# Performance work log

Hardware: AMD Instinct MI355X
Metric: run time of the kernel (lower is better)

## Reference

```python
import jax, jax.numpy as jnp
import numpy as np

BOUND = 1.0
GRID = 128
DENSITY_SCALE = 1.0
DENSITY_THRESH = 0.01
T_THRESH = 1e-3
BG_COLOR = 1.0
N_RAYS = 65536
N_STEPS = 128


def setup_inputs() -> dict:
    key = jax.random.key(0)
    ks = jax.random.split(key, 7)
    N, S = N_RAYS, N_STEPS
    # ray origins inside the AABB, directions unit-norm
    rays_o = (jax.random.uniform(ks[0], (N, 3)) - 0.5) * 1.0
    d = jax.random.normal(ks[1], (N, 3))
    rays_d = d / jnp.linalg.norm(d, axis=-1, keepdims=True)
    sigmas = jax.random.uniform(ks[2], (N, S)) * 2.0      # raw densities at samples
    rgbs = jax.random.uniform(ks[3], (N, S, 3))           # albedo at samples
    sun_v = jax.random.uniform(ks[4], (N, S))             # sun visibility (shadow)
    sky_color = jax.random.uniform(ks[5], (N, S, 3))      # ambient sky color
    nears = jnp.full((N,), 0.2, dtype=jnp.float32)
    fars = jnp.full((N,), 2.0, dtype=jnp.float32)
    density_grid = jax.random.uniform(ks[6], (GRID, GRID, GRID))  # occupancy grid
    return dict(rays_o=rays_o, rays_d=rays_d, sigmas=sigmas, rgbs=rgbs,
                sun_v=sun_v, sky_color=sky_color, nears=nears, fars=fars,
                density_grid=density_grid)


def reference(rays_o, rays_d, sigmas, rgbs, sun_v, sky_color, nears, fars, density_grid):
    N, S = sigmas.shape
    # --- march: uniform samples in [near, far] (dt_gamma = 0) ---
    dt = (fars - nears) / S                                        # [N]
    t = nears[:, None] + (jnp.arange(S, dtype=sigmas.dtype) + 0.5) * dt[:, None]  # [N,S]
    xyz = rays_o[:, None, :] + t[..., None] * rays_d[:, None, :]   # [N,S,3]
    # --- occupancy-grid lookup (density_bitfield test) ---
    idx = jnp.clip(((xyz + BOUND) / (2.0 * BOUND) * GRID).astype(jnp.int32), 0, GRID - 1)
    occ = density_grid[idx[..., 0], idx[..., 1], idx[..., 2]] > DENSITY_THRESH  # [N,S]
    inside = jnp.all(jnp.abs(xyz) < BOUND, axis=-1)                # AABB clip
    sig = jnp.where(occ & inside, sigmas * DENSITY_SCALE, 0.0)     # skip empty space
    # --- shading: irradiance = sun_v + (1 - sun_v) * sky_color ---
    irr = sun_v[..., None] + (1.0 - sun_v[..., None]) * sky_color  # [N,S,3]
    rgb = rgbs * irr
    # --- alpha compositing with early termination ---
    tau = sig * dt[:, None]                                        # optical depth per step
    T = jnp.exp(-(jnp.cumsum(tau, axis=-1) - tau))                 # exclusive transmittance
    alpha = 1.0 - jnp.exp(-tau)
    w = jnp.where(T > T_THRESH, alpha * T, 0.0)                    # early-termination mask
    weights_sum = w.sum(-1)                                        # [N]
    depth = (w * t).sum(-1)                                        # [N]
    image = jnp.einsum('ns,nsc->nc', w, rgb) + (1.0 - weights_sum)[:, None] * BG_COLOR
    depth = jnp.clip(depth - nears, 0.0) / (fars - nears)
    return image, depth, weights_sum
```

## Files before the change

kernel.cpp:

```cpp
#include <hip/hip_runtime.h>


#define NRAYS  65536
#define NSTEPS 128
#define GRIDN  128

typedef float v2f __attribute__((ext_vector_type(2)));

__global__ __launch_bounds__(256, 4) void nerf_render_kernel(
    const float* __restrict__ rays_o,
    const float* __restrict__ rays_d,
    const float* __restrict__ sigmas,
    const float* __restrict__ rgbs,
    const float* __restrict__ sun_v,
    const float* __restrict__ sky,
    const float* __restrict__ nears,
    const float* __restrict__ fars,
    const float* __restrict__ grid,
    float* __restrict__ out)
{
    const int tid  = blockIdx.x * blockDim.x + threadIdx.x;
    const int ray  = tid >> 6;
    const int lane = threadIdx.x & 63;
    if (ray >= NRAYS) return;

    const float nearv = nears[ray];
    const float farv  = fars[ray];
    const float dt    = (farv - nearv) * (1.0f / NSTEPS);

    const float ox = rays_o[ray * 3 + 0];
    const float oy = rays_o[ray * 3 + 1];
    const float oz = rays_o[ray * 3 + 2];
    const float dx = rays_d[ray * 3 + 0];
    const float dy = rays_d[ray * 3 + 1];
    const float dz = rays_d[ray * 3 + 2];

    const int  s0   = 2 * lane;
    const long base = (long)ray * NSTEPS + s0;

    const v2f sg  = *(const v2f*)(sigmas + base);
    const v2f sv  = *(const v2f*)(sun_v  + base);
    const v2f r01 = *(const v2f*)(rgbs + base * 3);
    const v2f r23 = *(const v2f*)(rgbs + base * 3 + 2);
    const v2f r45 = *(const v2f*)(rgbs + base * 3 + 4);
    const v2f k01 = *(const v2f*)(sky  + base * 3);
    const v2f k23 = *(const v2f*)(sky  + base * 3 + 2);
    const v2f k45 = *(const v2f*)(sky  + base * 3 + 4);

    float t_[2], tau_[2], cr_[2], cg_[2], cb_[2];
    const float rr_[2] = { r01[0], r23[1] };
    const float rg_[2] = { r01[1], r45[0] };
    const float rb_[2] = { r23[0], r45[1] };
    const float kr_[2] = { k01[0], k23[1] };
    const float kg_[2] = { k01[1], k45[0] };
    const float kb_[2] = { k23[0], k45[1] };

    #pragma unroll
    for (int j = 0; j < 2; ++j) {
        const int s = s0 + j;
        const float t = __fadd_rn(nearv, __fmul_rn((float)s + 0.5f, dt));
        const float x = __fadd_rn(ox, __fmul_rn(t, dx));
        const float y = __fadd_rn(oy, __fmul_rn(t, dy));
        const float z = __fadd_rn(oz, __fmul_rn(t, dz));

        int ix = (int)__fmul_rn(__fadd_rn(x, 1.0f), 64.0f);
        int iy = (int)__fmul_rn(__fadd_rn(y, 1.0f), 64.0f);
        int iz = (int)__fmul_rn(__fadd_rn(z, 1.0f), 64.0f);
        ix = min(max(ix, 0), GRIDN - 1);
        iy = min(max(iy, 0), GRIDN - 1);
        iz = min(max(iz, 0), GRIDN - 1);
        const float g = grid[((long)ix * GRIDN + iy) * GRIDN + iz];

        const bool inside = (fabsf(x) < 1.0f) & (fabsf(y) < 1.0f) & (fabsf(z) < 1.0f);
        const bool occ    = (g > 0.01f) & inside;

        const float sig = occ ? sg[j] : 0.0f;

        const float s_v = sv[j];
        cr_[j] = rr_[j] * (s_v + (1.0f - s_v) * kr_[j]);
        cg_[j] = rg_[j] * (s_v + (1.0f - s_v) * kg_[j]);
        cb_[j] = rb_[j] * (s_v + (1.0f - s_v) * kb_[j]);

        t_[j]   = t;
        tau_[j] = sig * dt;
    }

    const float pair = tau_[0] + tau_[1];
    float incl = pair;
    #pragma unroll
    for (int off = 1; off < 64; off <<= 1) {
        const float u = __shfl_up(incl, off);
        if (lane >= off) incl += u;
    }
    const float eLane = incl - pair;
    const float excl_[2] = { eLane, eLane + tau_[0] };

    float wsum = 0.0f, dsum = 0.0f, ir = 0.0f, ig = 0.0f, ib = 0.0f;
    #pragma unroll
    for (int j = 0; j < 2; ++j) {
        const float T     = expf(-excl_[j]);
        const float alpha = 1.0f - expf(-tau_[j]);
        const float w     = (T > 1e-3f) ? alpha * T : 0.0f;
        wsum += w; dsum += w * t_[j];
        ir += w * cr_[j]; ig += w * cg_[j]; ib += w * cb_[j];
    }

    #pragma unroll
    for (int off = 32; off > 0; off >>= 1) {
        wsum += __shfl_xor(wsum, off);
        dsum += __shfl_xor(dsum, off);
        ir   += __shfl_xor(ir, off);
        ig   += __shfl_xor(ig, off);
        ib   += __shfl_xor(ib, off);
    }

    if (lane == 0) {
        const float bgw = 1.0f - wsum;
        out[ray * 3 + 0] = ir + bgw;
        out[ray * 3 + 1] = ig + bgw;
        out[ray * 3 + 2] = ib + bgw;
        out[3 * NRAYS + ray] = fmaxf(dsum - nearv, 0.0f) / (farv - nearv);
        out[4 * NRAYS + ray] = wsum;
    }
}

extern "C" void kernel_launch(void* const* d_in, const int* in_sizes, int n_in,
                              void* d_out, int out_size, void* d_ws, size_t ws_size,
                              hipStream_t stream) {
    const float* rays_o = (const float*)d_in[0];
    const float* rays_d = (const float*)d_in[1];
    const float* sigmas = (const float*)d_in[2];
    const float* rgbs   = (const float*)d_in[3];
    const float* sun_v  = (const float*)d_in[4];
    const float* sky    = (const float*)d_in[5];
    const float* nears  = (const float*)d_in[6];
    const float* fars   = (const float*)d_in[7];
    const float* grid   = (const float*)d_in[8];
    float* out = (float*)d_out;

    const int threads = 256;
    const int blocks  = (NRAYS * 64) / threads;
    nerf_render_kernel<<<blocks, threads, 0, stream>>>(
        rays_o, rays_d, sigmas, rgbs, sun_v, sky, nears, fars, grid, out);
}
```

Measured before the change: 289.0 us.

## Process eight rays per wave with double-buffered prefetch and nontemporal loads

Each wave now handles eight consecutive rays instead of one, with A/B register sets so loads for the next ray (including the grid gather) are issued before compositing the current one. Streaming per-sample inputs use nontemporal loads to avoid polluting cache. This cuts the block count by 8x and is meant to hide memory latency via software pipelining, at the cost of more registers per thread and less wave-level parallelism.

```diff
diff --git a/kernel.cpp b/kernel.cpp
--- a/kernel.cpp
+++ b/kernel.cpp
@@ -4,8 +4,109 @@
 #define NRAYS  65536
 #define NSTEPS 128
 #define GRIDN  128
+#define RPW    8
+#define WPB    4
 
 typedef float v2f __attribute__((ext_vector_type(2)));
+
+__device__ __forceinline__ v2f ntload2(const float* p) {
+    return __builtin_nontemporal_load((const v2f*)p);
+}
+
+#define PREFETCH(rayi, P)                                                      \
+  do {                                                                         \
+    const int _ray = (rayi);                                                   \
+    P##_near = nears[_ray];  P##_far = fars[_ray];                             \
+    P##_ox = rays_o[_ray*3+0]; P##_oy = rays_o[_ray*3+1]; P##_oz = rays_o[_ray*3+2]; \
+    P##_dx = rays_d[_ray*3+0]; P##_dy = rays_d[_ray*3+1]; P##_dz = rays_d[_ray*3+2]; \
+    const float _dt = (P##_far - P##_near) * (1.0f/NSTEPS);                    \
+    _Pragma("unroll")                                                          \
+    for (int _j = 0; _j < 2; ++_j) {                                           \
+      const float _t = __fadd_rn(P##_near, __fmul_rn((float)(s0+_j)+0.5f, _dt)); \
+      const float _x = __fadd_rn(P##_ox, __fmul_rn(_t, P##_dx));               \
+      const float _y = __fadd_rn(P##_oy, __fmul_rn(_t, P##_dy));               \
+      const float _z = __fadd_rn(P##_oz, __fmul_rn(_t, P##_dz));               \
+      int _ix = (int)__fmul_rn(__fadd_rn(_x, 1.0f), 64.0f);                    \
+      int _iy = (int)__fmul_rn(__fadd_rn(_y, 1.0f), 64.0f);                    \
+      int _iz = (int)__fmul_rn(__fadd_rn(_z, 1.0f), 64.0f);                    \
+      _ix = min(max(_ix,0),GRIDN-1); _iy = min(max(_iy,0),GRIDN-1); _iz = min(max(_iz,0),GRIDN-1); \
+      const float _g = grid[((long)_ix*GRIDN + _iy)*GRIDN + _iz];              \
+      if (_j == 0) P##_g0 = _g; else P##_g1 = _g;                              \
+    }                                                                          \
+    const long _base = (long)_ray * NSTEPS + s0;                               \
+    P##_sg  = ntload2(sigmas + _base);                                         \
+    P##_sv  = ntload2(sun_v  + _base);                                         \
+    P##_r01 = ntload2(rgbs + _base*3);                                         \
+    P##_r23 = ntload2(rgbs + _base*3 + 2);                                     \
+    P##_r45 = ntload2(rgbs + _base*3 + 4);                                     \
+    P##_k01 = ntload2(sky  + _base*3);                                         \
+    P##_k23 = ntload2(sky  + _base*3 + 2);                                     \
+    P##_k45 = ntload2(sky  + _base*3 + 4);                                     \
+  } while (0)
+
+#define COMPUTE(rayi, P)                                                       \
+  do {                                                                         \
+    const int _ray = (rayi);                                                   \
+    const float _dt = (P##_far - P##_near) * (1.0f/NSTEPS);                    \
+    float t_[2], tau_[2], cr_[2], cg_[2], cb_[2];                              \
+    const float rr_[2] = { P##_r01[0], P##_r23[1] };                           \
+    const float rg_[2] = { P##_r01[1], P##_r45[0] };                           \
+    const float rb_[2] = { P##_r23[0], P##_r45[1] };                           \
+    const float kr_[2] = { P##_k01[0], P##_k23[1] };                           \
+    const float kg_[2] = { P##_k01[1], P##_k45[0] };                           \
+    const float kb_[2] = { P##_k23[0], P##_k45[1] };                           \
+    const float g_[2]  = { P##_g0, P##_g1 };                                   \
+    _Pragma("unroll")                                                          \
+    for (int _j = 0; _j < 2; ++_j) {                                           \
+      const float _t = __fadd_rn(P##_near, __fmul_rn((float)(s0+_j)+0.5f, _dt)); \
+      const float _x = __fadd_rn(P##_ox, __fmul_rn(_t, P##_dx));               \
+      const float _y = __fadd_rn(P##_oy, __fmul_rn(_t, P##_dy));               \
+      const float _z = __fadd_rn(P##_oz, __fmul_rn(_t, P##_dz));               \
+      const bool _inside = (fabsf(_x) < 1.0f) & (fabsf(_y) < 1.0f) & (fabsf(_z) < 1.0f); \
+      const bool _occ    = (g_[_j] > 0.01f) & _inside;                         \
+      const float _sig = _occ ? P##_sg[_j] : 0.0f;                             \
+      const float _sv  = P##_sv[_j];                                           \
+      cr_[_j] = rr_[_j] * (_sv + (1.0f - _sv) * kr_[_j]);                      \
+      cg_[_j] = rg_[_j] * (_sv + (1.0f - _sv) * kg_[_j]);                      \
+      cb_[_j] = rb_[_j] * (_sv + (1.0f - _sv) * kb_[_j]);                      \
+      t_[_j]   = _t;                                                           \
+      tau_[_j] = _sig * _dt;                                                   \
+    }                                                                          \
+    const float _pair = tau_[0] + tau_[1];                                     \
+    float _incl = _pair;                                                       \
+    _Pragma("unroll")                                                          \
+    for (int _off = 1; _off < 64; _off <<= 1) {                                \
+      const float _u = __shfl_up(_incl, _off);                                 \
+      if (lane >= _off) _incl += _u;                                           \
+    }                                                                          \
+    const float _eLane = _incl - _pair;                                        \
+    const float excl_[2] = { _eLane, _eLane + tau_[0] };                       \
+    float _ws = 0.0f, _ds = 0.0f, _ir = 0.0f, _ig = 0.0f, _ib = 0.0f;          \
+    _Pragma("unroll")                                                          \
+    for (int _j = 0; _j < 2; ++_j) {                                           \
+      const float _T     = expf(-excl_[_j]);                                   \
+      const float _alpha = 1.0f - expf(-tau_[_j]);                             \
+      const float _w     = (_T > 1e-3f) ? _alpha * _T : 0.0f;                  \
+      _ws += _w; _ds += _w * t_[_j];                                           \
+      _ir += _w * cr_[_j]; _ig += _w * cg_[_j]; _ib += _w * cb_[_j];           \
+    }                                                                          \
+    _Pragma("unroll")                                                          \
+    for (int _off = 32; _off > 0; _off >>= 1) {                                \
+      _ws += __shfl_xor(_ws, _off);                                            \
+      _ds += __shfl_xor(_ds, _off);                                            \
+      _ir += __shfl_xor(_ir, _off);                                            \
+      _ig += __shfl_xor(_ig, _off);                                            \
+      _ib += __shfl_xor(_ib, _off);                                            \
+    }                                                                          \
+    if (lane == 0) {                                                           \
+      const float _bgw = 1.0f - _ws;                                           \
+      out[_ray*3 + 0] = _ir + _bgw;                                            \
+      out[_ray*3 + 1] = _ig + _bgw;                                            \
+      out[_ray*3 + 2] = _ib + _bgw;                                            \
+      out[3*NRAYS + _ray] = fmaxf(_ds - P##_near, 0.0f) / (P##_far - P##_near);\
+      out[4*NRAYS + _ray] = _ws;                                               \
+    }                                                                          \
+  } while (0)
 
 __global__ __launch_bounds__(256, 4) void nerf_render_kernel(
     const float* __restrict__ rays_o,
@@ -19,109 +120,26 @@
     const float* __restrict__ grid,
     float* __restrict__ out)
 {
-    const int tid  = blockIdx.x * blockDim.x + threadIdx.x;
-    const int ray  = tid >> 6;
     const int lane = threadIdx.x & 63;
-    if (ray >= NRAYS) return;
+    const int wloc = __builtin_amdgcn_readfirstlane(threadIdx.x >> 6);
+    const int wave = blockIdx.x * WPB + wloc;
+    const int ray0 = wave * RPW;
+    const int s0   = 2 * lane;
 
-    const float nearv = nears[ray];
-    const float farv  = fars[ray];
-    const float dt    = (farv - nearv) * (1.0f / NSTEPS);
+    v2f A_sg, A_sv, A_r01, A_r23, A_r45, A_k01, A_k23, A_k45;
+    float A_g0, A_g1, A_near, A_far, A_ox, A_oy, A_oz, A_dx, A_dy, A_dz;
+    v2f B_sg, B_sv, B_r01, B_r23, B_r45, B_k01, B_k23, B_k45;
+    float B_g0, B_g1, B_near, B_far, B_ox, B_oy, B_oz, B_dx, B_dy, B_dz;
 
-    const float ox = rays_o[ray * 3 + 0];
-    const float oy = rays_o[ray * 3 + 1];
-    const float oz = rays_o[ray * 3 + 2];
-    const float dx = rays_d[ray * 3 + 0];
-    const float dy = rays_d[ray * 3 + 1];
-    const float dz = rays_d[ray * 3 + 2];
-
-    const int  s0   = 2 * lane;
-    const long base = (long)ray * NSTEPS + s0;
-
-    const v2f sg  = *(const v2f*)(sigmas + base);
-    const v2f sv  = *(const v2f*)(sun_v  + base);
-    const v2f r01 = *(const v2f*)(rgbs + base * 3);
-    const v2f r23 = *(const v2f*)(rgbs + base * 3 + 2);
-    const v2f r45 = *(const v2f*)(rgbs + base * 3 + 4);
-    const v2f k01 = *(const v2f*)(sky  + base * 3);
-    const v2f k23 = *(const v2f*)(sky  + base * 3 + 2);
-    const v2f k45 = *(const v2f*)(sky  + base * 3 + 4);
-
-    float t_[2], tau_[2], cr_[2], cg_[2], cb_[2];
-    const float rr_[2] = { r01[0], r23[1] };
-    const float rg_[2] = { r01[1], r45[0] };
-    const float rb_[2] = { r23[0], r45[1] };
-    const float kr_[2] = { k01[0], k23[1] };
-    const float kg_[2] = { k01[1], k45[0] };
-    const float kb_[2] = { k23[0], k45[1] };
-
-    #pragma unroll
-    for (int j = 0; j < 2; ++j) {
-        const int s = s0 + j;
-        const float t = __fadd_rn(nearv, __fmul_rn((float)s + 0.5f, dt));
-        const float x = __fadd_rn(ox, __fmul_rn(t, dx));
-        const float y = __fadd_rn(oy, __fmul_rn(t, dy));
-        const float z = __fadd_rn(oz, __fmul_rn(t, dz));
-
-        int ix = (int)__fmul_rn(__fadd_rn(x, 1.0f), 64.0f);
-        int iy = (int)__fmul_rn(__fadd_rn(y, 1.0f), 64.0f);
-        int iz = (int)__fmul_rn(__fadd_rn(z, 1.0f), 64.0f);
-        ix = min(max(ix, 0), GRIDN - 1);
-        iy = min(max(iy, 0), GRIDN - 1);
-        iz = min(max(iz, 0), GRIDN - 1);
-        const float g = grid[((long)ix * GRIDN + iy) * GRIDN + iz];
-
-        const bool inside = (fabsf(x) < 1.0f) & (fabsf(y) < 1.0f) & (fabsf(z) < 1.0f);
-        const bool occ    = (g > 0.01f) & inside;
-
-        const float sig = occ ? sg[j] : 0.0f;
-
-        const float s_v = sv[j];
-        cr_[j] = rr_[j] * (s_v + (1.0f - s_v) * kr_[j]);
-        cg_[j] = rg_[j] * (s_v + (1.0f - s_v) * kg_[j]);
-        cb_[j] = rb_[j] * (s_v + (1.0f - s_v) * kb_[j]);
-
-        t_[j]   = t;
-        tau_[j] = sig * dt;
-    }
-
-    const float pair = tau_[0] + tau_[1];
-    float incl = pair;
-    #pragma unroll
-    for (int off = 1; off < 64; off <<= 1) {
-        const float u = __shfl_up(incl, off);
-        if (lane >= off) incl += u;
-    }
-    const float eLane = incl - pair;
-    const float excl_[2] = { eLane, eLane + tau_[0] };
-
-    float wsum = 0.0f, dsum = 0.0f, ir = 0.0f, ig = 0.0f, ib = 0.0f;
-    #pragma unroll
-    for (int j = 0; j < 2; ++j) {
-        const float T     = expf(-excl_[j]);
-        const float alpha = 1.0f - expf(-tau_[j]);
-        const float w     = (T > 1e-3f) ? alpha * T : 0.0f;
-        wsum += w; dsum += w * t_[j];
-        ir += w * cr_[j]; ig += w * cg_[j]; ib += w * cb_[j];
-    }
-
-    #pragma unroll
-    for (int off = 32; off > 0; off >>= 1) {
-        wsum += __shfl_xor(wsum, off);
-        dsum += __shfl_xor(dsum, off);
-        ir   += __shfl_xor(ir, off);
-        ig   += __shfl_xor(ig, off);
-        ib   += __shfl_xor(ib, off);
-    }
-
-    if (lane == 0) {
-        const float bgw = 1.0f - wsum;
-        out[ray * 3 + 0] = ir + bgw;
-        out[ray * 3 + 1] = ig + bgw;
-        out[ray * 3 + 2] = ib + bgw;
-        out[3 * NRAYS + ray] = fmaxf(dsum - nearv, 0.0f) / (farv - nearv);
-        out[4 * NRAYS + ray] = wsum;
-    }
+    PREFETCH(ray0 + 0, A);
+    PREFETCH(ray0 + 1, B);  COMPUTE(ray0 + 0, A);
+    PREFETCH(ray0 + 2, A);  COMPUTE(ray0 + 1, B);
+    PREFETCH(ray0 + 3, B);  COMPUTE(ray0 + 2, A);
+    PREFETCH(ray0 + 4, A);  COMPUTE(ray0 + 3, B);
+    PREFETCH(ray0 + 5, B);  COMPUTE(ray0 + 4, A);
+    PREFETCH(ray0 + 6, A);  COMPUTE(ray0 + 5, B);
+    PREFETCH(ray0 + 7, B);  COMPUTE(ray0 + 6, A);
+                            COMPUTE(ray0 + 7, B);
 }
 
 extern "C" void kernel_launch(void* const* d_in, const int* in_sizes, int n_in,
@@ -139,7 +157,7 @@
     float* out = (float*)d_out;
 
     const int threads = 256;
-    const int blocks  = (NRAYS * 64) / threads;
+    const int blocks  = NRAYS / (WPB * RPW);
     nerf_render_kernel<<<blocks, threads, 0, stream>>>(
         rays_o, rays_d, sigmas, rgbs, sun_v, sky, nears, fars, grid, out);
 }
```

Result: no change. 291.7 us (+0.9%).
